# Performance work log

Hardware: AMD Instinct MI355X
Metric: run time of the kernel (lower is better)

## Reference

```python
import jax, jax.numpy as jnp
import numpy as np
from jax import lax

DT, TAU = 16.67, 40.0
ALPHA = DT / TAU
ONE_MINUS_ALPHA = 1.0 - ALPHA


def setup_inputs() -> dict:
    key = jax.random.key(0)
    k = jax.random.split(key, 6)
    B, T, D, H = 256, 2048, 32, 64
    x = jax.random.normal(k[0], (B, T, D), dtype=jnp.float32)
    seq_lengths = jax.random.randint(k[1], (B,), 0, T, dtype=jnp.int32)
    W_in = jax.random.normal(k[2], (H, D), dtype=jnp.float32) * (1.0 / np.sqrt(D))
    b_in = jax.random.normal(k[3], (H,), dtype=jnp.float32) * 0.01
    W_hh = jax.random.normal(k[4], (H, H), dtype=jnp.float32) * (1.0 / np.sqrt(H))
    b_hh = jax.random.normal(k[5], (H,), dtype=jnp.float32) * 0.01
    return {"x": x, "seq_lengths": seq_lengths, "W_in": W_in, "b_in": b_in,
            "W_hh": W_hh, "b_hh": b_hh}


def reference(x, seq_lengths, W_in, b_in, W_hh, b_hh):
    B, T, D = x.shape
    H = W_hh.shape[0]
    # mask[b, t] = (t < seq_lengths[b]); forward value is identical either way
    # (the torch masking only stops gradients past seq end).
    mask = (jnp.arange(T)[None, :] < seq_lengths[:, None]).astype(x.dtype)  # [B,T]
    # Precompute input projection for all timesteps in one GEMM: [B,T,H]
    x_proj = jnp.einsum('btd,hd->bth', x, W_in) + b_in
    h0 = jnp.zeros((B, H), dtype=x.dtype)

    def step(h, inp):
        xp_t, m_t = inp  # [B,H], [B,1]
        pre = xp_t + h @ W_hh.T + b_hh
        h_new = jax.nn.relu(h * ONE_MINUS_ALPHA + pre * ALPHA)
        # hidden*mask + detach(hidden)*(1-mask): same value, gradient gated by mask
        h_new = h_new * m_t + lax.stop_gradient(h_new) * (1.0 - m_t)
        return h_new, h_new

    xs = (jnp.transpose(x_proj, (1, 0, 2)), mask.T[:, :, None])  # time-major
    h_last, outs = lax.scan(step, h0, xs)
    outputs = jnp.transpose(outs, (1, 0, 2))  # [B,T,H]
    return outputs, h_last
```

## Files before the change

kernel.cpp:

```cpp
#include <hip/hip_runtime.h>


#define Bb 256
#define Tt 2048
#define Dd 32
#define Hh 64

typedef float v2f __attribute__((ext_vector_type(2)));

static constexpr float ALPHA = (float)(16.67 / 40.0);
static constexpr float OMA   = 1.0f - ALPHA;

static __device__ inline v2f vfma2(v2f a, v2f b, v2f c) {
#if __has_builtin(__builtin_elementwise_fma)
    return __builtin_elementwise_fma(a, b, c);
#else
    v2f r; r.x = fmaf(a.x, b.x, c.x); r.y = fmaf(a.y, b.y, c.y); return r;
#endif
}

__global__ __launch_bounds__(256) void ctrnn_xproj(
    const float* __restrict__ x,
    const float* __restrict__ W_in,
    float* __restrict__ out)
{
    __shared__ alignas(16) float xs[128 * Dd];
    const int tid  = threadIdx.x;
    const int lane = tid & 63;
    const int wave = tid >> 6;
    const int b    = blockIdx.x >> 4;
    const int tile = blockIdx.x & 15;
    const int t0   = tile * 128;

    const float4* xsrc = reinterpret_cast<const float4*>(
        x + (size_t)b * Tt * Dd + (size_t)t0 * Dd);
    float4* xdst = reinterpret_cast<float4*>(xs);
#pragma unroll
    for (int r = 0; r < 4; ++r) xdst[r * 256 + tid] = xsrc[r * 256 + tid];

    v2f w[16];
    const v2f* wrow = reinterpret_cast<const v2f*>(W_in + lane * Dd);
#pragma unroll
    for (int j = 0; j < 16; ++j) w[j] = wrow[j];

    __syncthreads();

    float* ob = out + (size_t)b * Tt * Hh + (size_t)t0 * Hh;
    const int lt0 = wave * 32;
#pragma unroll 2
    for (int i = 0; i < 32; ++i) {
        const float4* xr = reinterpret_cast<const float4*>(xs + (lt0 + i) * Dd);
        v2f a01 = {0.f, 0.f}, a23 = {0.f, 0.f};
#pragma unroll
        for (int j = 0; j < 8; ++j) {
            const float4 xv = xr[j];
            const v2f x01 = {xv.x, xv.y};
            const v2f x23 = {xv.z, xv.w};
            a01 = vfma2(w[2 * j + 0], x01, a01);
            a23 = vfma2(w[2 * j + 1], x23, a23);
        }
        ob[(size_t)(lt0 + i) * Hh + lane] = (a01.x + a01.y) + (a23.x + a23.y);
    }
}

__global__ __launch_bounds__(64) void ctrnn_recur(
    const float* __restrict__ b_in,
    const float* __restrict__ W_hh,
    const float* __restrict__ b_hh,
    float* __restrict__ out)
{
    const int b    = blockIdx.x;
    const int lane = threadIdx.x;

    float4 w4[16];
    const float4* wr = reinterpret_cast<const float4*>(W_hh + lane * Hh);
#pragma unroll
    for (int j = 0; j < 16; ++j) w4[j] = wr[j];

    const float cb = ALPHA * (b_in[lane] + b_hh[lane]);

    float* ob = out + (size_t)b * Tt * Hh + lane;

    float xp[8];
#pragma unroll
    for (int j = 0; j < 8; ++j) xp[j] = ob[(size_t)j * Hh];

    float* op       = ob;
    const float* lp = ob + 8 * (size_t)Hh;

    float hold = 0.0f;
    for (int t = 0; t < Tt; t += 8) {
#pragma unroll
        for (int j = 0; j < 8; ++j) {
            const int hb = __float_as_int(hold);
            float s0 = 0.f, s1 = 0.f, s2 = 0.f, s3 = 0.f;
#pragma unroll
            for (int k = 0; k < 16; ++k) {
                const float h0 = __int_as_float(__builtin_amdgcn_readlane(hb, 4 * k + 0));
                const float h1 = __int_as_float(__builtin_amdgcn_readlane(hb, 4 * k + 1));
                const float h2 = __int_as_float(__builtin_amdgcn_readlane(hb, 4 * k + 2));
                const float h3 = __int_as_float(__builtin_amdgcn_readlane(hb, 4 * k + 3));
                s0 = fmaf(w4[k].x, h0, s0);
                s1 = fmaf(w4[k].y, h1, s1);
                s2 = fmaf(w4[k].z, h2, s2);
                s3 = fmaf(w4[k].w, h3, s3);
            }
            const float sum  = ((s0 + s2) + (s1 + s3)) + xp[j];
            const float hnew = fmaxf(fmaf(ALPHA, sum, fmaf(OMA, hold, cb)), 0.0f);

            *op = hnew;
            op += Hh;
            hold = hnew;

            xp[j] = *lp;
            lp += Hh;
        }
    }
    out[(size_t)Bb * Tt * Hh + (size_t)b * Hh + lane] = hold;
}

extern "C" void kernel_launch(void* const* d_in, const int* in_sizes, int n_in,
                              void* d_out, int out_size, void* d_ws, size_t ws_size,
                              hipStream_t stream) {
    const float* x    = (const float*)d_in[0];
    const float* W_in = (const float*)d_in[2];
    const float* b_in = (const float*)d_in[3];
    const float* W_hh = (const float*)d_in[4];
    const float* b_hh = (const float*)d_in[5];
    float* out = (float*)d_out;

    ctrnn_xproj<<<dim3(Bb * 16), dim3(256), 0, stream>>>(x, W_in, out);
    ctrnn_recur<<<dim3(Bb), dim3(64), 0, stream>>>(b_in, W_hh, b_hh, out);
}
```

Measured before the change: 664.8 us.

## Fuse input projection into recurrence kernel and broadcast hidden state via LDS

```diff
diff --git a/kernel.cpp b/kernel.cpp
--- a/kernel.cpp
+++ b/kernel.cpp
@@ -5,8 +5,11 @@
 #define Tt 2048
 #define Dd 32
 #define Hh 64
+#define TILE 128
+#define NT (Tt / TILE)
 
 typedef float v2f __attribute__((ext_vector_type(2)));
+typedef float v4f __attribute__((ext_vector_type(4)));
 
 static constexpr float ALPHA = (float)(16.67 / 40.0);
 static constexpr float OMA   = 1.0f - ALPHA;
@@ -19,51 +22,9 @@
 #endif
 }
 
-__global__ __launch_bounds__(256) void ctrnn_xproj(
+__global__ __launch_bounds__(64, 1) void ctrnn_fused(
     const float* __restrict__ x,
     const float* __restrict__ W_in,
-    float* __restrict__ out)
-{
-    __shared__ alignas(16) float xs[128 * Dd];
-    const int tid  = threadIdx.x;
-    const int lane = tid & 63;
-    const int wave = tid >> 6;
-    const int b    = blockIdx.x >> 4;
-    const int tile = blockIdx.x & 15;
-    const int t0   = tile * 128;
-
-    const float4* xsrc = reinterpret_cast<const float4*>(
-        x + (size_t)b * Tt * Dd + (size_t)t0 * Dd);
-    float4* xdst = reinterpret_cast<float4*>(xs);
-#pragma unroll
-    for (int r = 0; r < 4; ++r) xdst[r * 256 + tid] = xsrc[r * 256 + tid];
-
-    v2f w[16];
-    const v2f* wrow = reinterpret_cast<const v2f*>(W_in + lane * Dd);
-#pragma unroll
-    for (int j = 0; j < 16; ++j) w[j] = wrow[j];
-
-    __syncthreads();
-
-    float* ob = out + (size_t)b * Tt * Hh + (size_t)t0 * Hh;
-    const int lt0 = wave * 32;
-#pragma unroll 2
-    for (int i = 0; i < 32; ++i) {
-        const float4* xr = reinterpret_cast<const float4*>(xs + (lt0 + i) * Dd);
-        v2f a01 = {0.f, 0.f}, a23 = {0.f, 0.f};
-#pragma unroll
-        for (int j = 0; j < 8; ++j) {
-            const float4 xv = xr[j];
-            const v2f x01 = {xv.x, xv.y};
-            const v2f x23 = {xv.z, xv.w};
-            a01 = vfma2(w[2 * j + 0], x01, a01);
-            a23 = vfma2(w[2 * j + 1], x23, a23);
-        }
-        ob[(size_t)(lt0 + i) * Hh + lane] = (a01.x + a01.y) + (a23.x + a23.y);
-    }
-}
-
-__global__ __launch_bounds__(64) void ctrnn_recur(
     const float* __restrict__ b_in,
     const float* __restrict__ W_hh,
     const float* __restrict__ b_hh,
@@ -72,48 +33,106 @@
     const int b    = blockIdx.x;
     const int lane = threadIdx.x;
 
-    float4 w4[16];
-    const float4* wr = reinterpret_cast<const float4*>(W_hh + lane * Hh);
+    __shared__ alignas(16) float xstage[TILE * Dd];
+    __shared__ alignas(16) float xpb[TILE * Hh];
+    __shared__ alignas(16) float hs[Hh];
+
+    v2f w[16];
+    const v2f* wir = reinterpret_cast<const v2f*>(W_in + lane * Dd);
+#pragma unroll
+    for (int j = 0; j < 16; ++j) w[j] = wir[j];
+
+    v4f w4[16];
+    const v4f* wr = reinterpret_cast<const v4f*>(W_hh + lane * Hh);
 #pragma unroll
     for (int j = 0; j < 16; ++j) w4[j] = wr[j];
 
     const float cb = ALPHA * (b_in[lane] + b_hh[lane]);
 
-    float* ob = out + (size_t)b * Tt * Hh + lane;
+    const float4* xsrc_base = reinterpret_cast<const float4*>(
+        x + (size_t)b * Tt * Dd);
+    float* op = out + (size_t)b * Tt * Hh + lane;
 
-    float xp[8];
-#pragma unroll
-    for (int j = 0; j < 8; ++j) xp[j] = ob[(size_t)j * Hh];
+    const v4f*  h4    = reinterpret_cast<const v4f*>(hs);
+    float4*     xdst4 = reinterpret_cast<float4*>(xstage);
 
-    float* op       = ob;
-    const float* lp = ob + 8 * (size_t)Hh;
+    hs[lane] = 0.0f;
+    v4f q0  = h4[2],  q1  = h4[3],  q2  = h4[4],  q3  = h4[5];
+    v4f q4  = h4[6],  q5  = h4[7],  q6  = h4[8],  q7  = h4[9];
+    v4f q8  = h4[10], q9  = h4[11], q10 = h4[12], q11 = h4[13];
+    v4f q12 = h4[14], q13 = h4[15];
 
     float hold = 0.0f;
-    for (int t = 0; t < Tt; t += 8) {
+    float pre  = cb;
+
+    for (int n = 0; n < NT; ++n) {
+        const float4* xsrc = xsrc_base + (size_t)n * TILE * (Dd / 4);
 #pragma unroll
-        for (int j = 0; j < 8; ++j) {
-            const int hb = __float_as_int(hold);
-            float s0 = 0.f, s1 = 0.f, s2 = 0.f, s3 = 0.f;
+        for (int i = 0; i < 16; ++i)
+            xdst4[i * 64 + lane] = xsrc[i * 64 + lane];
+
+#pragma unroll 2
+        for (int i = 0; i < TILE; ++i) {
+            const float4* xr = reinterpret_cast<const float4*>(xstage + i * Dd);
+            v2f a01 = {0.f, 0.f}, a23 = {0.f, 0.f};
 #pragma unroll
-            for (int k = 0; k < 16; ++k) {
-                const float h0 = __int_as_float(__builtin_amdgcn_readlane(hb, 4 * k + 0));
-                const float h1 = __int_as_float(__builtin_amdgcn_readlane(hb, 4 * k + 1));
-                const float h2 = __int_as_float(__builtin_amdgcn_readlane(hb, 4 * k + 2));
-                const float h3 = __int_as_float(__builtin_amdgcn_readlane(hb, 4 * k + 3));
-                s0 = fmaf(w4[k].x, h0, s0);
-                s1 = fmaf(w4[k].y, h1, s1);
-                s2 = fmaf(w4[k].z, h2, s2);
-                s3 = fmaf(w4[k].w, h3, s3);
+            for (int j = 0; j < 8; ++j) {
+                const float4 xv = xr[j];
+                const v2f x01 = {xv.x, xv.y};
+                const v2f x23 = {xv.z, xv.w};
+                a01 = vfma2(w[2 * j + 0], x01, a01);
+                a23 = vfma2(w[2 * j + 1], x23, a23);
             }
-            const float sum  = ((s0 + s2) + (s1 + s3)) + xp[j];
-            const float hnew = fmaxf(fmaf(ALPHA, sum, fmaf(OMA, hold, cb)), 0.0f);
+            xpb[i * Hh + lane] = (a01.x + a01.y) + (a23.x + a23.y);
+        }
 
-            *op = hnew;
-            op += Hh;
-            hold = hnew;
+        for (int tb = 0; tb < TILE; tb += 8) {
+            float xp[8];
+#pragma unroll
+            for (int j = 0; j < 8; ++j) xp[j] = xpb[(tb + j) * Hh + lane];
 
-            xp[j] = *lp;
-            lp += Hh;
+#pragma unroll
+            for (int j = 0; j < 8; ++j) {
+                const int hb = __float_as_int(hold);
+                float s0 = 0.f, s1 = 0.f, s2 = 0.f, s3 = 0.f;
+#pragma unroll
+                for (int k = 0; k < 2; ++k) {
+                    const float h0 = __int_as_float(__builtin_amdgcn_readlane(hb, 4 * k + 0));
+                    const float h1 = __int_as_float(__builtin_amdgcn_readlane(hb, 4 * k + 1));
+                    const float h2 = __int_as_float(__builtin_amdgcn_readlane(hb, 4 * k + 2));
+                    const float h3 = __int_as_float(__builtin_amdgcn_readlane(hb, 4 * k + 3));
+                    s0 = fmaf(w4[k][0], h0, s0);
+                    s1 = fmaf(w4[k][1], h1, s1);
+                    s2 = fmaf(w4[k][2], h2, s2);
+                    s3 = fmaf(w4[k][3], h3, s3);
+                }
+                v2f acc01 = {s0, s1}, acc23 = {s2, s3};
+#define QPK(K, Q)                                                              \
+                acc01 = vfma2(__builtin_shufflevector(w4[K], w4[K], 0, 1),     \
+                              __builtin_shufflevector((Q), (Q), 0, 1), acc01); \
+                acc23 = vfma2(__builtin_shufflevector(w4[K], w4[K], 2, 3),     \
+                              __builtin_shufflevector((Q), (Q), 2, 3), acc23);
+                QPK( 2, q0)  QPK( 3, q1)  QPK( 4, q2)  QPK( 5, q3)
+                QPK( 6, q4)  QPK( 7, q5)  QPK( 8, q6)  QPK( 9, q7)
+                QPK(10, q8)  QPK(11, q9)  QPK(12, q10) QPK(13, q11)
+                QPK(14, q12) QPK(15, q13)
+#undef QPK
+                const v2f tt     = acc01 + acc23;
+                const float sum  = (tt.x + tt.y) + xp[j];
+                const float hnew = fmaxf(fmaf(ALPHA, sum, pre), 0.0f);
+
+                hs[lane] = hnew;
+                q0  = h4[2];  q1  = h4[3];  q2  = h4[4];  q3  = h4[5];
+                q4  = h4[6];  q5  = h4[7];  q6  = h4[8];  q7  = h4[9];
+                q8  = h4[10]; q9  = h4[11]; q10 = h4[12]; q11 = h4[13];
+                q12 = h4[14]; q13 = h4[15];
+                __builtin_amdgcn_sched_barrier(0);
+
+                *op = hnew;
+                op += Hh;
+                hold = hnew;
+                pre  = fmaf(OMA, hnew, cb);
+            }
         }
     }
     out[(size_t)Bb * Tt * Hh + (size_t)b * Hh + lane] = hold;
@@ -129,6 +148,5 @@
     const float* b_hh = (const float*)d_in[5];
     float* out = (float*)d_out;
 
-    ctrnn_xproj<<<dim3(Bb * 16), dim3(256), 0, stream>>>(x, W_in, out);
-    ctrnn_recur<<<dim3(Bb), dim3(64), 0, stream>>>(b_in, W_hh, b_hh, out);
+    ctrnn_fused<<<dim3(Bb), dim3(64), 0, stream>>>(x, W_in, b_in, W_hh, b_hh, out);
 }
```

New measurement: 634.7 us. 1.05x faster.
